# Optimization experiments

Hardware: AMD Instinct MI355X
Metric: run time of the kernel (lower is better)

## Reference

```python
import jax, jax.numpy as jnp
import numpy as np


def setup_inputs() -> dict:
    key = jax.random.key(0)
    ks = jax.random.split(key, 8)
    B, Tq, S, H = 32, 4, 2048, 1024
    return {
        "query": jax.random.normal(ks[0], (B, Tq, H), dtype=jnp.float32),
        "keys": jax.random.normal(ks[1], (S, B, 2 * H), dtype=jnp.float32),
        "Wa_w": jax.random.normal(ks[2], (H, H), dtype=jnp.float32) * 0.02,
        "Wa_b": jax.random.normal(ks[3], (H,), dtype=jnp.float32) * 0.02,
        "Ua_w": jax.random.normal(ks[4], (H, 2 * H), dtype=jnp.float32) * 0.02,
        "Ua_b": jax.random.normal(ks[5], (H,), dtype=jnp.float32) * 0.02,
        "Va_w": jax.random.normal(ks[6], (1, H), dtype=jnp.float32) * 0.02,
        "Va_b": jax.random.normal(ks[7], (1,), dtype=jnp.float32) * 0.02,
    }


def reference(query, keys, Wa_w, Wa_b, Ua_w, Ua_b, Va_w, Va_b):
    # query: [B, Tq, H] -> last step [B, 1, H]
    q = query[:, -1:, :]
    # keys: [S, B, 2H] -> [B, S, 2H]
    k = jnp.transpose(keys, (1, 0, 2))
    # Additive attention scores: Va(tanh(Wa(q) + Ua(k)))
    wq = q @ Wa_w.T + Wa_b                      # [B, 1, H]
    uk = k @ Ua_w.T + Ua_b                      # [B, S, H]
    scores = jnp.tanh(wq + uk) @ Va_w.T + Va_b  # [B, S, 1]
    scores = jnp.transpose(scores, (0, 2, 1))   # [B, 1, S]
    weights = jax.nn.softmax(scores, axis=-1)   # [B, 1, S]
    context = jnp.einsum('bqs,bsd->bqd', weights, k)  # [B, 1, 2H]
    return (context, weights)
```

## Files before the change

### kernel.cpp

```cpp
#include <hip/hip_runtime.h>
#include <hip/hip_bf16.h>

typedef __attribute__((ext_vector_type(4))) float f32x4;
typedef __attribute__((ext_vector_type(8))) short short8;

#define B_   32
#define S_   2048
#define H_   1024
#define D2_  2048
#define BM   256
#define BN   256
#define BK   32
#define NKT  64
#define TILE_SH 8192


__device__ __forceinline__ short f2bf(float f) {
  unsigned u = __float_as_uint(f);
  u = (u + 0x7fffu + ((u >> 16) & 1u)) >> 16;
  return (short)u;
}

__device__ __forceinline__ float bf2f(short s) {
  return __uint_as_float(((unsigned)(unsigned short)s) << 16);
}

__device__ __forceinline__ short8 cvt8(f32x4 a, f32x4 b) {
  short8 o;
  o[0] = f2bf(a.x); o[1] = f2bf(a.y); o[2] = f2bf(a.z); o[3] = f2bf(a.w);
  o[4] = f2bf(b.x); o[5] = f2bf(b.y); o[6] = f2bf(b.z); o[7] = f2bf(b.w);
  return o;
}

__device__ __forceinline__ float fast_tanh(float x) {
  float e = __builtin_amdgcn_exp2f(x * 2.885390081777927f);
  return 1.0f - 2.0f * __builtin_amdgcn_rcpf(e + 1.0f);
}

__device__ __forceinline__ void gload16(const short* g, short* l) {
  __builtin_amdgcn_global_load_lds((const __attribute__((address_space(1))) void*)g,
                                   (__attribute__((address_space(3))) void*)l, 16, 0, 0);
}

__global__ void k_convert_ua(const float* __restrict__ src, short* __restrict__ dst) {
  int idx = blockIdx.x * 256 + threadIdx.x;
  int unit = idx & 1023;
  int kts  = (idx >> 10) & 63;
  int nt   = idx >> 16;
  int row  = unit >> 2;
  int sl   = unit & 3;
  int q    = sl ^ ((row >> 1) & 3);
  const float* s = src + (size_t)(nt * 256 + row) * D2_ + kts * 32 + q * 8;
  f32x4 a = *(const f32x4*)s;
  f32x4 b = *(const f32x4*)(s + 4);
  *(short8*)(dst + (size_t)idx * 8) = cvt8(a, b);
}

__global__ void k_convert_keys(const float* __restrict__ src, short* __restrict__ dst) {
  int idx = blockIdx.x * 256 + threadIdx.x;
  int unit = idx & 1023;
  int kts  = (idx >> 10) & 63;
  int mt   = idx >> 16;
  int row  = unit >> 2;
  int sl   = unit & 3;
  int q    = sl ^ ((row >> 1) & 3);
  const float* s = src + (size_t)(mt * 256 + row) * D2_ + kts * 32 + q * 8;
  f32x4 a = *(const f32x4*)s;
  f32x4 b = *(const f32x4*)(s + 4);
  *(short8*)(dst + (size_t)idx * 8) = cvt8(a, b);
}

__global__ void k_wq(const float* __restrict__ query, const float* __restrict__ Wa_w,
                     const float* __restrict__ Wa_b, const float* __restrict__ Ua_b,
                     float* __restrict__ wqb) {
  int b = blockIdx.x;
  int hc = blockIdx.y;
  int t = threadIdx.x;
  __shared__ float q[H_];
  for (int i = t; i < H_; i += 256) q[i] = query[(size_t)b * (4 * H_) + 3 * H_ + i];
  __syncthreads();
  int h = hc * 128 + (t >> 1);
  int kh = (t & 1) * 512;
  const float* wr = Wa_w + (size_t)h * H_ + kh;
  float acc = 0.f;
  #pragma unroll 8
  for (int k = 0; k < 512; k += 4) {
    f32x4 wv = *(const f32x4*)(wr + k);
    acc += wv.x * q[kh + k] + wv.y * q[kh + k + 1] + wv.z * q[kh + k + 2] + wv.w * q[kh + k + 3];
  }
  acc += __shfl_xor(acc, 1);
  if ((t & 1) == 0) wqb[b * H_ + h] = acc + Wa_b[h] + Ua_b[h];
}

#define MCL16(mb, AF)                                                                             \
  __builtin_amdgcn_s_setprio(1);                                                                  \
  _Pragma("unroll")                                                                               \
  for (int n = 0; n < 4; ++n) {                                                                   \
    _Pragma("unroll")                                                                             \
    for (int i = 0; i < 4; ++i)                                                                   \
      acc[(mb) + i][n] =                                                                          \
          __builtin_amdgcn_mfma_f32_16x16x32_bf16(AF[i], bf[n], acc[(mb) + i][n], 0, 0, 0);       \
  }                                                                                               \
  __builtin_amdgcn_s_setprio(0);

__global__ __launch_bounds__(512, 2) void k_gemm_score(
    const short* __restrict__ keys_bf, const short* __restrict__ uab_t,
    const float* __restrict__ wqb, const float* __restrict__ va,
    float* __restrict__ scores_p) {
  __shared__ short As[3][TILE_SH];
  __shared__ short Bs[3][TILE_SH];

  const int bid = blockIdx.x;
  const int g = (bid & 7) * 128 + (bid >> 3);
  const int mt = g >> 2;
  const int nt = g & 3;
  const int r0 = mt * BM;
  const int h0 = nt * BN;

  const int t = threadIdx.x;
  const int lane = t & 63;
  const int w = t >> 6;
  const int wm = w >> 2;
  const int wn = w & 3;

  f32x4 acc[8][4] = {};

  const short* abase = keys_bf + (size_t)mt * (NKT * TILE_SH) + t * 8;
  const short* bbase = uab_t  + (size_t)nt * (NKT * TILE_SH) + t * 8;
  const int wu = w * 512;

  const int lr = lane & 15;
  const int lq = lane >> 4;
  const int slot = lq ^ ((lr >> 1) & 3);
  const int aoff = (wm * 128 + lr) * 32 + slot * 8;
  const int boff = (wn * 64 + lr) * 32 + slot * 8;

  {
    gload16(abase,                  &As[0][wu]);
    gload16(abase + 4096,           &As[0][4096 + wu]);
    gload16(bbase,                  &Bs[0][wu]);
    gload16(bbase + 4096,           &Bs[0][4096 + wu]);
    gload16(abase + TILE_SH,        &As[1][wu]);
    gload16(abase + TILE_SH + 4096, &As[1][4096 + wu]);
    gload16(bbase + TILE_SH,        &Bs[1][wu]);
    gload16(bbase + TILE_SH + 4096, &Bs[1][4096 + wu]);
    asm volatile("s_waitcnt vmcnt(4)" ::: "memory");
    __builtin_amdgcn_s_barrier();
  }

  short8 bf[4], af0[4], af1[4];
  int cur = 0;

  #pragma unroll 1
  for (int kts = 0; kts < NKT; ++kts) {
    int stg = cur + 2; if (stg >= 3) stg -= 3;
    const short* Ac = &As[cur][0];
    const short* Bc = &Bs[cur][0];

    #pragma unroll
    for (int n = 0; n < 4; ++n) bf[n] = *(const short8*)&Bc[boff + n * 512];
    #pragma unroll
    for (int i = 0; i < 4; ++i) af0[i] = *(const short8*)&Ac[aoff + i * 512];
    #pragma unroll
    for (int i = 0; i < 4; ++i) af1[i] = *(const short8*)&Ac[aoff + 2048 + i * 512];

    if (kts < NKT - 2) {
      const short* an = abase + (size_t)(kts + 2) * TILE_SH;
      const short* bn = bbase + (size_t)(kts + 2) * TILE_SH;
      gload16(an,        &As[stg][wu]);
      gload16(an + 4096, &As[stg][4096 + wu]);
      gload16(bn,        &Bs[stg][wu]);
      gload16(bn + 4096, &Bs[stg][4096 + wu]);
    }

    MCL16(0, af0)
    MCL16(4, af1)

    if (kts < NKT - 2) {
      asm volatile("s_waitcnt vmcnt(4)" ::: "memory");
    } else if (kts == NKT - 2) {
      asm volatile("s_waitcnt vmcnt(0)" ::: "memory");
    }
    if (kts < NKT - 1) __builtin_amdgcn_s_barrier();

    cur = (cur == 2) ? 0 : cur + 1;
  }

  const int lgrp = lane >> 4;
  const int lc = lane & 15;
  float vah[4];
  #pragma unroll
  for (int n = 0; n < 4; ++n) vah[n] = va[h0 + wn * 64 + n * 16 + lc];
  #pragma unroll
  for (int m = 0; m < 8; ++m) {
    #pragma unroll
    for (int reg = 0; reg < 4; ++reg) {
      int row = wm * 128 + m * 16 + lgrp * 4 + reg;
      int r = r0 + row;
      int bb = r & (B_ - 1);
      const float* wrow = wqb + bb * H_ + h0 + wn * 64 + lc;
      float s = 0.f;
      #pragma unroll
      for (int n = 0; n < 4; ++n)
        s += vah[n] * fast_tanh(acc[m][n][reg] + wrow[n * 16]);
      s += __shfl_xor(s, 1);
      s += __shfl_xor(s, 2);
      s += __shfl_xor(s, 4);
      s += __shfl_xor(s, 8);
      if (lc == 0) scores_p[(size_t)r * 16 + nt * 4 + wn] = s;
    }
  }
}

__global__ __launch_bounds__(512, 2) void k_gemm_rs(
    const float* __restrict__ keys, const short* __restrict__ uab_t,
    const float* __restrict__ wqb, const float* __restrict__ va,
    float* __restrict__ scores_p) {
  __shared__ short As[2][TILE_SH];
  __shared__ short Bs[2][TILE_SH];
  const int bid = blockIdx.x;
  const int g = (bid & 7) * 128 + (bid >> 3);
  const int mt = g >> 2;
  const int nt = g & 3;
  const int r0 = mt * BM;
  const int h0 = nt * BN;
  const int t = threadIdx.x;
  const int lane = t & 63;
  const int w = t >> 6;
  const int wm = w >> 2;
  const int wn = w & 3;
  f32x4 acc[8][4] = {};
  const int arow = t >> 1;
  const int hh = t & 1;
  const float* abase = keys + (size_t)(r0 + arow) * D2_ + hh * 16;
  int awoff[2];
  #pragma unroll
  for (int j = 0; j < 2; ++j)
    awoff[j] = arow * 32 + (((2 * hh + j) ^ ((arow >> 1) & 3)) << 3);
  const short* bbase = uab_t + (size_t)nt * NKT * TILE_SH + t * 8;
  const int wu = w * 512;
  const int lr = lane & 15;
  const int lq = lane >> 4;
  const int slot = lq ^ ((lr >> 1) & 3);
  const int aoff = (wm * 128 + lr) * 32 + slot * 8;
  const int boff = (wn * 64 + lr) * 32 + slot * 8;
  short8 bf[4], af0[4], af1[4];
  {
    f32x4 v0 = *(const f32x4*)(abase);
    f32x4 v1 = *(const f32x4*)(abase + 4);
    f32x4 v2 = *(const f32x4*)(abase + 8);
    f32x4 v3 = *(const f32x4*)(abase + 12);
    *(short8*)&As[0][awoff[0]] = cvt8(v0, v1);
    *(short8*)&As[0][awoff[1]] = cvt8(v2, v3);
    gload16(bbase,        &Bs[0][wu]);
    gload16(bbase + 4096, &Bs[0][4096 + wu]);
    asm volatile("s_waitcnt vmcnt(0) lgkmcnt(0)" ::: "memory");
    __builtin_amdgcn_s_barrier();
  }
  #pragma unroll 1
  for (int kts = 0; kts < NKT; ++kts) {
    const int cb = kts & 1;
    const bool stage = (kts < NKT - 1);
    const float* anext = abase + (kts + 1) * BK;
    const short* bnext = bbase + (size_t)(kts + 1) * TILE_SH;
    short* Anb = &As[cb ^ 1][0];
    short* Bnb = &Bs[cb ^ 1][0];
    const short* Ac = As[cb];
    const short* Bc = Bs[cb];

    #pragma unroll
    for (int n = 0; n < 4; ++n) bf[n] = *(const short8*)&Bc[boff + n * 512];
    #pragma unroll
    for (int i = 0; i < 4; ++i) af0[i] = *(const short8*)&Ac[aoff + i * 512];
    #pragma unroll
    for (int i = 0; i < 4; ++i) af1[i] = *(const short8*)&Ac[aoff + 2048 + i * 512];
    f32x4 v0, v1, v2, v3;
    if (stage) {
      v0 = *(const f32x4*)(anext);
      v1 = *(const f32x4*)(anext + 4);
      v2 = *(const f32x4*)(anext + 8);
      v3 = *(const f32x4*)(anext + 12);
      gload16(bnext,        Bnb + wu);
      gload16(bnext + 4096, Bnb + 4096 + wu);
    }
    MCL16(0, af0)
    MCL16(4, af1)
    __builtin_amdgcn_s_barrier();
    if (stage) {
      *(short8*)&Anb[awoff[0]] = cvt8(v0, v1);
      *(short8*)&Anb[awoff[1]] = cvt8(v2, v3);
    }
    asm volatile("s_waitcnt vmcnt(0) lgkmcnt(0)" ::: "memory");
    __builtin_amdgcn_s_barrier();
  }
  const int lgrp = lane >> 4;
  const int lc = lane & 15;
  float vah[4];
  #pragma unroll
  for (int n = 0; n < 4; ++n) vah[n] = va[h0 + wn * 64 + n * 16 + lc];
  #pragma unroll
  for (int m = 0; m < 8; ++m) {
    #pragma unroll
    for (int reg = 0; reg < 4; ++reg) {
      int row = wm * 128 + m * 16 + lgrp * 4 + reg;
      int r = r0 + row;
      int bb = r & (B_ - 1);
      const float* wrow = wqb + bb * H_ + h0 + wn * 64 + lc;
      float s = 0.f;
      #pragma unroll
      for (int n = 0; n < 4; ++n)
        s += vah[n] * fast_tanh(acc[m][n][reg] + wrow[n * 16]);
      s += __shfl_xor(s, 1);
      s += __shfl_xor(s, 2);
      s += __shfl_xor(s, 4);
      s += __shfl_xor(s, 8);
      if (lc == 0) scores_p[(size_t)r * 16 + nt * 4 + wn] = s;
    }
  }
}

__global__ void k_softmax(const float* __restrict__ scores_p, float* __restrict__ out) {
  int b = blockIdx.x;
  int t = threadIdx.x;
  __shared__ float sc[S_];
  __shared__ float red[4];
  float lmax = -3.4e38f;
  #pragma unroll
  for (int i = 0; i < 8; ++i) {
    int s = t + i * 256;
    const float* p = scores_p + ((size_t)s * B_ + b) * 16;
    f32x4 p0 = *(const f32x4*)p;
    f32x4 p1 = *(const f32x4*)(p + 4);
    f32x4 p2 = *(const f32x4*)(p + 8);
    f32x4 p3 = *(const f32x4*)(p + 12);
    f32x4 ps = p0 + p1 + p2 + p3;
    float v = ps.x + ps.y + ps.z + ps.w;
    sc[s] = v;
    lmax = fmaxf(lmax, v);
  }
  #pragma unroll
  for (int o = 32; o >= 1; o >>= 1) lmax = fmaxf(lmax, __shfl_xor(lmax, o));
  if ((t & 63) == 0) red[t >> 6] = lmax;
  __syncthreads();
  float gmax = fmaxf(fmaxf(red[0], red[1]), fmaxf(red[2], red[3]));
  __syncthreads();
  float lsum = 0.f;
  #pragma unroll
  for (int i = 0; i < 8; ++i) {
    int s = t + i * 256;
    float e = __builtin_amdgcn_exp2f((sc[s] - gmax) * 1.4426950408889634f);
    sc[s] = e;
    lsum += e;
  }
  #pragma unroll
  for (int o = 32; o >= 1; o >>= 1) lsum += __shfl_xor(lsum, o);
  if ((t & 63) == 0) red[t >> 6] = lsum;
  __syncthreads();
  float inv = 1.0f / (red[0] + red[1] + red[2] + red[3]);
  for (int i = 0; i < 8; ++i) {
    int s = t + i * 256;
    out[(size_t)65536 + b * S_ + s] = sc[s] * inv;
  }
}

__global__ __launch_bounds__(256) void k_ctx_partial_bf2(const short* __restrict__ keys_bf,
                                                         const float* __restrict__ wts,
                                                         float* __restrict__ cp) {
  const int ktp = blockIdx.x;
  const int mtc = blockIdx.y;
  const int t = threadIdx.x;
  const int cg = t >> 5;
  const int b = t & 31;
  const int kts = ktp * 2 + (cg >> 2);
  const int slot = (cg & 3) ^ ((b >> 1) & 3);
  const float* wbase = wts + (size_t)b * S_ + mtc * 128;
  f32x4 accA = {}, accB = {};
  #pragma unroll 2
  for (int c = 0; c < 16; ++c) {
    const short* tb = keys_bf + ((size_t)((mtc * 16 + c) * 64 + kts)) * TILE_SH + (slot << 3);
    f32x4 w0 = *(const f32x4*)(wbase + c * 8);
    f32x4 w1 = *(const f32x4*)(wbase + c * 8 + 4);
    float wg[8] = {w0.x, w0.y, w0.z, w0.w, w1.x, w1.y, w1.z, w1.w};
    #pragma unroll
    for (int s8 = 0; s8 < 8; ++s8) {
      short8 v = *(const short8*)(tb + (s8 * 32 + b) * 32);
      float wgt = wg[s8];
      accA.x += wgt * bf2f(v[0]); accA.y += wgt * bf2f(v[1]);
      accA.z += wgt * bf2f(v[2]); accA.w += wgt * bf2f(v[3]);
      accB.x += wgt * bf2f(v[4]); accB.y += wgt * bf2f(v[5]);
      accB.z += wgt * bf2f(v[6]); accB.w += wgt * bf2f(v[7]);
    }
  }
  float* o = cp + ((size_t)mtc * B_ + b) * D2_ + ktp * 64 + (cg & 3) * 8 + (cg >> 2) * 32;
  *(f32x4*)o = accA;
  *(f32x4*)(o + 4) = accB;
}

__global__ void k_ctx_partial(const float* __restrict__ keys, const float* __restrict__ wts,
                              float* __restrict__ cp) {
  int b = blockIdx.x;
  int dc = blockIdx.y;
  int scn = blockIdx.z;
  int t = threadIdx.x;
  __shared__ float wl[256];
  int s0 = scn * 256;
  wl[t] = wts[b * S_ + s0 + t];
  __syncthreads();
  int d = dc * 1024 + t * 4;
  f32x4 acc = {};
  #pragma unroll 4
  for (int i = 0; i < 256; ++i) {
    int s = s0 + i;
    f32x4 kv = *(const f32x4*)(keys + ((size_t)s * B_ + b) * D2_ + d);
    acc += kv * wl[i];
  }
  *(f32x4*)(cp + ((size_t)scn * B_ + b) * D2_ + d) = acc;
}

__global__ void k_ctx_reduce(const float* __restrict__ cp, float* __restrict__ out, int np) {
  int i = blockIdx.x * 256 + threadIdx.x;
  float s = 0.f;
  for (int j = 0; j < np; ++j) s += cp[(size_t)j * 65536 + i];
  out[i] = s;
}

extern "C" void kernel_launch(void* const* d_in, const int* in_sizes, int n_in,
                              void* d_out, int out_size, void* d_ws, size_t ws_size,
                              hipStream_t stream) {
  const float* query = (const float*)d_in[0];
  const float* keys  = (const float*)d_in[1];
  const float* Wa_w  = (const float*)d_in[2];
  const float* Wa_b  = (const float*)d_in[3];
  const float* Ua_w  = (const float*)d_in[4];
  const float* Ua_b  = (const float*)d_in[5];
  const float* Va_w  = (const float*)d_in[6];
  float* out = (float*)d_out;
  char* ws = (char*)d_ws;

  const size_t KEYS_BF_BYTES = 268435456ull;
  const size_t TAIL = 16ull * 1024 * 1024;
  bool big = ws_size >= KEYS_BF_BYTES + TAIL;

  if (big) {
    short* keys_bf = (short*)ws;
    char* base = ws + KEYS_BF_BYTES;
    short* uab_t = (short*)(base);
    float* wqb = (float*)(base + 4u * 1024 * 1024);
    float* sp  = (float*)(base + 4u * 1024 * 1024 + 128 * 1024);
    float* cp  = (float*)(base + 8u * 1024 * 1024 + 256 * 1024);

    hipLaunchKernelGGL(k_convert_ua, dim3(1024), dim3(256), 0, stream, Ua_w, uab_t);
    hipLaunchKernelGGL(k_convert_keys, dim3(65536), dim3(256), 0, stream, keys, keys_bf);
    hipLaunchKernelGGL(k_wq, dim3(32, 8), dim3(256), 0, stream, query, Wa_w, Wa_b, Ua_b, wqb);
    hipLaunchKernelGGL(k_gemm_score, dim3(1024), dim3(512), 0, stream, keys_bf, uab_t, wqb, Va_w, sp);
    hipLaunchKernelGGL(k_softmax, dim3(32), dim3(256), 0, stream, sp, out);
    hipLaunchKernelGGL(k_ctx_partial_bf2, dim3(32, 16), dim3(256), 0, stream, keys_bf, out + 65536, cp);
    hipLaunchKernelGGL(k_ctx_reduce, dim3(256), dim3(256), 0, stream, cp, out, 16);
  } else {
    short* uab_t = (short*)(ws);
    float* wqb = (float*)(ws + 4u * 1024 * 1024);
    float* sp  = (float*)(ws + 4u * 1024 * 1024 + 128 * 1024);
    float* cp  = (float*)(ws + 8u * 1024 * 1024 + 256 * 1024);

    hipLaunchKernelGGL(k_convert_ua, dim3(1024), dim3(256), 0, stream, Ua_w, uab_t);
    hipLaunchKernelGGL(k_wq, dim3(32, 8), dim3(256), 0, stream, query, Wa_w, Wa_b, Ua_b, wqb);
    hipLaunchKernelGGL(k_gemm_rs, dim3(1024), dim3(512), 0, stream, keys, uab_t, wqb, Va_w, sp);
    hipLaunchKernelGGL(k_softmax, dim3(32), dim3(256), 0, stream, sp, out);
    hipLaunchKernelGGL(k_ctx_partial, dim3(32, 2, 8), dim3(256), 0, stream, keys, out + 65536, cp);
    hipLaunchKernelGGL(k_ctx_reduce, dim3(256), dim3(256), 0, stream, cp, out, 8);
  }
}
```

Before: 477.9 us.

## Load B operand fragments directly from global into registers, drop B LDS staging

```diff
diff --git a/kernel.cpp b/kernel.cpp
--- a/kernel.cpp
+++ b/kernel.cpp
@@ -92,23 +92,51 @@
   if ((t & 1) == 0) wqb[b * H_ + h] = acc + Wa_b[h] + Ua_b[h];
 }
 
-#define MCL16(mb, AF)                                                                             \
+#define MCL16(mb, AF, BF)                                                                         \
   __builtin_amdgcn_s_setprio(1);                                                                  \
   _Pragma("unroll")                                                                               \
   for (int n = 0; n < 4; ++n) {                                                                   \
     _Pragma("unroll")                                                                             \
     for (int i = 0; i < 4; ++i)                                                                   \
       acc[(mb) + i][n] =                                                                          \
-          __builtin_amdgcn_mfma_f32_16x16x32_bf16(AF[i], bf[n], acc[(mb) + i][n], 0, 0, 0);       \
+          __builtin_amdgcn_mfma_f32_16x16x32_bf16(AF[i], BF[n], acc[(mb) + i][n], 0, 0, 0);       \
   }                                                                                               \
   __builtin_amdgcn_s_setprio(0);
+
+#define KT_BODY(KT, BFC, BFN)                                                                     \
+  {                                                                                               \
+    const short* Ac = &As[cur][0];                                                                \
+    _Pragma("unroll")                                                                             \
+    for (int i = 0; i < 4; ++i) af0[i] = *(const short8*)&Ac[aoff + i * 512];                     \
+    _Pragma("unroll")                                                                             \
+    for (int i = 0; i < 4; ++i) af1[i] = *(const short8*)&Ac[aoff + 2048 + i * 512];              \
+    if ((KT) + 1 < NKT) {                                                                         \
+      const short* bp = bgf + (size_t)((KT) + 1) * TILE_SH;                                       \
+      _Pragma("unroll")                                                                           \
+      for (int n = 0; n < 4; ++n) BFN[n] = *(const short8*)(bp + n * 512);                        \
+    }                                                                                             \
+    if ((KT) + 2 < NKT) {                                                                         \
+      int stg = cur + 2; if (stg >= 3) stg -= 3;                                                  \
+      const short* an = abase + (size_t)((KT) + 2) * TILE_SH;                                     \
+      gload16(an,        &As[stg][wu]);                                                           \
+      gload16(an + 4096, &As[stg][4096 + wu]);                                                    \
+    }                                                                                             \
+    MCL16(0, af0, BFC)                                                                            \
+    MCL16(4, af1, BFC)                                                                            \
+    if ((KT) + 2 < NKT) {                                                                         \
+      asm volatile("s_waitcnt vmcnt(6)" ::: "memory");                                            \
+    } else if ((KT) + 1 < NKT) {                                                                  \
+      asm volatile("s_waitcnt vmcnt(4)" ::: "memory");                                            \
+    }                                                                                             \
+    if ((KT) + 1 < NKT) __builtin_amdgcn_s_barrier();                                             \
+    cur = (cur == 2) ? 0 : cur + 1;                                                               \
+  }
 
 __global__ __launch_bounds__(512, 2) void k_gemm_score(
     const short* __restrict__ keys_bf, const short* __restrict__ uab_t,
     const float* __restrict__ wqb, const float* __restrict__ va,
     float* __restrict__ scores_p) {
   __shared__ short As[3][TILE_SH];
-  __shared__ short Bs[3][TILE_SH];
 
   const int bid = blockIdx.x;
   const int g = (bid & 7) * 128 + (bid >> 3);
@@ -126,7 +154,6 @@
   f32x4 acc[8][4] = {};
 
   const short* abase = keys_bf + (size_t)mt * (NKT * TILE_SH) + t * 8;
-  const short* bbase = uab_t  + (size_t)nt * (NKT * TILE_SH) + t * 8;
   const int wu = w * 512;
 
   const int lr = lane & 15;
@@ -134,56 +161,26 @@
   const int slot = lq ^ ((lr >> 1) & 3);
   const int aoff = (wm * 128 + lr) * 32 + slot * 8;
   const int boff = (wn * 64 + lr) * 32 + slot * 8;
+  const short* bgf = uab_t + (size_t)nt * (NKT * TILE_SH) + boff;
+
+  short8 af0[4], af1[4], bfX[4], bfY[4];
 
   {
+    #pragma unroll
+    for (int n = 0; n < 4; ++n) bfX[n] = *(const short8*)(bgf + n * 512);
     gload16(abase,                  &As[0][wu]);
     gload16(abase + 4096,           &As[0][4096 + wu]);
-    gload16(bbase,                  &Bs[0][wu]);
-    gload16(bbase + 4096,           &Bs[0][4096 + wu]);
     gload16(abase + TILE_SH,        &As[1][wu]);
     gload16(abase + TILE_SH + 4096, &As[1][4096 + wu]);
-    gload16(bbase + TILE_SH,        &Bs[1][wu]);
-    gload16(bbase + TILE_SH + 4096, &Bs[1][4096 + wu]);
-    asm volatile("s_waitcnt vmcnt(4)" ::: "memory");
+    asm volatile("s_waitcnt vmcnt(2)" ::: "memory");
     __builtin_amdgcn_s_barrier();
   }
 
-  short8 bf[4], af0[4], af1[4];
   int cur = 0;
-
   #pragma unroll 1
-  for (int kts = 0; kts < NKT; ++kts) {
-    int stg = cur + 2; if (stg >= 3) stg -= 3;
-    const short* Ac = &As[cur][0];
-    const short* Bc = &Bs[cur][0];
-
-    #pragma unroll
-    for (int n = 0; n < 4; ++n) bf[n] = *(const short8*)&Bc[boff + n * 512];
-    #pragma unroll
-    for (int i = 0; i < 4; ++i) af0[i] = *(const short8*)&Ac[aoff + i * 512];
-    #pragma unroll
-    for (int i = 0; i < 4; ++i) af1[i] = *(const short8*)&Ac[aoff + 2048 + i * 512];
-
-    if (kts < NKT - 2) {
-      const short* an = abase + (size_t)(kts + 2) * TILE_SH;
-      const short* bn = bbase + (size_t)(kts + 2) * TILE_SH;
-      gload16(an,        &As[stg][wu]);
-      gload16(an + 4096, &As[stg][4096 + wu]);
-      gload16(bn,        &Bs[stg][wu]);
-      gload16(bn + 4096, &Bs[stg][4096 + wu]);
-    }
-
-    MCL16(0, af0)
-    MCL16(4, af1)
-
-    if (kts < NKT - 2) {
-      asm volatile("s_waitcnt vmcnt(4)" ::: "memory");
-    } else if (kts == NKT - 2) {
-      asm volatile("s_waitcnt vmcnt(0)" ::: "memory");
-    }
-    if (kts < NKT - 1) __builtin_amdgcn_s_barrier();
-
-    cur = (cur == 2) ? 0 : cur + 1;
+  for (int ktp = 0; ktp < NKT / 2; ++ktp) {
+    KT_BODY(2 * ktp,     bfX, bfY)
+    KT_BODY(2 * ktp + 1, bfY, bfX)
   }
 
   const int lgrp = lane >> 4;
@@ -283,8 +280,8 @@
       gload16(bnext,        Bnb + wu);
       gload16(bnext + 4096, Bnb + 4096 + wu);
     }
-    MCL16(0, af0)
-    MCL16(4, af1)
+    MCL16(0, af0, bf)
+    MCL16(4, af1, bf)
     __builtin_amdgcn_s_barrier();
     if (stage) {
       *(short8*)&Anb[awoff[0]] = cvt8(v0, v1);
```

Result: slower. 538.3 us (+12.7%).
